# Optimization experiments

Measured on AMD Instinct MI355X. Metric: run time of the kernel, lower is better.

The kernel has to match this reference:

```python
import jax, jax.numpy as jnp
import numpy as np

S, N, LAT, HID, NH, NLAYERS = 8, 128, 128, 384, 8, 6
HT, WT, DT = 128, 128, 128
DIN, DOUT, RAD, LEVELS, FED = 1169, 3 + 3 * 128, 3, 4, 64


def sincos1d(d, pos):
    # MAE-style 1d sincos embedding, d even -> [..., d]
    omega = 1.0 / (10000.0 ** (jnp.arange(d // 2, dtype=jnp.float32) / (d / 2.0)))
    ang = pos[..., None] * omega
    return jnp.concatenate([jnp.sin(ang), jnp.cos(ang)], axis=-1)


def flow_embed(f, Cd=FED):
    # get_3d_embedding(flows, 64, cat_coords=True) -> [..., 3*Cd+3] = 195
    div = jnp.arange(0, Cd, 2, dtype=jnp.float32) * (1000.0 / Cd)
    outs = []
    for a in range(3):
        ang = f[..., a, None] * div
        pe = jnp.stack([jnp.sin(ang), jnp.cos(ang)], axis=-1).reshape(f.shape[:-1] + (Cd,))
        outs.append(pe)
    return jnp.concatenate(outs + [f], axis=-1)


def avg_pool2(x):
    B, Sv, Cc, H, W = x.shape
    return x.reshape(B, Sv, Cc, H // 2, 2, W // 2, 2).mean(axis=(4, 6))


def pyramid(fm):
    pyr = [fm]
    for _ in range(LEVELS - 1):
        fm = avg_pool2(fm)
        pyr.append(fm)
    return pyr


def bilinear_sample(corr, xy):
    # corr: [B,S,N,H,W]; xy: [B,S,N,P,2] pixel coords (x indexes W, y indexes H); zero padding
    B, Sv, Nn, H, W = corr.shape
    cf = corr.reshape(B, Sv, Nn, H * W)
    x, y = xy[..., 0], xy[..., 1]
    x0f = jnp.floor(x); y0f = jnp.floor(y)
    wx, wy = x - x0f, y - y0f
    x0 = x0f.astype(jnp.int32); y0 = y0f.astype(jnp.int32)

    def gather(xi, yi):
        ok = ((xi >= 0) & (xi < W) & (yi >= 0) & (yi < H)).astype(cf.dtype)
        idx = jnp.clip(yi, 0, H - 1) * W + jnp.clip(xi, 0, W - 1)
        v = jnp.take_along_axis(cf, idx.reshape(B, Sv, Nn, -1), axis=-1).reshape(idx.shape)
        return v * ok

    v00 = gather(x0, y0); v01 = gather(x0 + 1, y0)
    v10 = gather(x0, y0 + 1); v11 = gather(x0 + 1, y0 + 1)
    return v00 * (1 - wx) * (1 - wy) + v01 * wx * (1 - wy) + v10 * (1 - wx) * wy + v11 * wx * wy


def corr_sample(pyr, targets, coords):
    # RAFT/CoTracker CorrBlock: per-level dense correlation then (2r+1)^2 window bilinear lookup
    d = jnp.arange(-RAD, RAD + 1, dtype=jnp.float32)
    delta = jnp.stack(jnp.meshgrid(d, d, indexing="ij"), axis=-1).reshape(-1, 2)  # [49,2]
    scale = 1.0 / jnp.sqrt(jnp.float32(targets.shape[-1]))
    outs = []
    for l, fm in enumerate(pyr):
        corr = jnp.einsum("bsnc,bschw->bsnhw", targets, fm) * scale
        xy = coords[..., None, :] / (2.0 ** l) + delta
        outs.append(bilinear_sample(corr, xy))
    return jnp.concatenate(outs, axis=-1)  # [B,S,N,196]


def layernorm(x, g, b):
    m = x.mean(-1, keepdims=True)
    v = x.var(-1, keepdims=True)
    return (x - m) / jnp.sqrt(v + 1e-5) * g + b


def attention(x, Wqkv, bq, Wo, bo):
    M, T, H = x.shape
    dh = H // NH
    qkv = (x @ Wqkv + bq).reshape(M, T, 3, NH, dh)
    q, k, v = qkv[:, :, 0], qkv[:, :, 1], qkv[:, :, 2]
    att = jax.nn.softmax(jnp.einsum("mthd,mshd->mhts", q, k) / jnp.sqrt(jnp.float32(dh)), axis=-1)
    o = jnp.einsum("mhts,mshd->mthd", att, v).reshape(M, T, H)
    return o @ Wo + bo


def updateformer(x, support, W_in, b_in, lnp, Wqkv, bqkv, Wo, bo, W1, b1, W2, b2, W_out, b_out, Ws, bs):
    # x: [B,N,T,DIN]; alternating time (over T) and space (over N) pre-LN transformer blocks
    B, Np, T, _ = x.shape
    sproj = support @ Ws + bs  # [100,HID]
    h = x @ W_in + b_in + sproj.mean(axis=0)
    for i in range(NLAYERS):
        g1, bb1, g2, bb2 = lnp[i, 0], lnp[i, 1], lnp[i, 2], lnp[i, 3]
        if i % 2 == 0:
            y = h.reshape(B * Np, T, HID)
        else:
            y = h.transpose(0, 2, 1, 3).reshape(B * T, Np, HID)
        y = y + attention(layernorm(y, g1, bb1), Wqkv[i], bqkv[i], Wo[i], bo[i])
        z = layernorm(y, g2, bb2)
        y = y + jax.nn.gelu(z @ W1[i] + b1[i], approximate=False) @ W2[i] + b2[i]
        if i % 2 == 0:
            h = y.reshape(B, Np, T, HID)
        else:
            h = y.reshape(B, T, Np, HID).transpose(0, 2, 1, 3)
    return h @ W_out + b_out, sproj[None]


def groupnorm1(x, g, b):
    m = x.mean(-1, keepdims=True)
    v = x.var(-1, keepdims=True)
    return (x - m) / jnp.sqrt(v + 1e-5) * g + b


def _forward(fmapXY, fmapYZ, fmapXZ, coords_init, vis_init, track_mask, feat_init, support_features,
             W_in, b_in, lnp, Wqkv, bqkv, Wo, bo, W1, b1, W2, b2, W_out, b_out, Ws, bs,
             gn_g, gn_b, Wu, bu, Wvis, bvis, iters):
    B, Sv, Cc, H, W = fmapXY.shape
    D = fmapXZ.shape[-2]
    Nn = coords_init.shape[2]
    coords = coords_init
    ffeats = [feat_init[..., k] for k in range(3)]
    pyrXY, pyrYZ, pyrXZ = pyramid(fmapXY), pyramid(fmapYZ), pyramid(fmapXZ)
    grid_size = jnp.array([H, W, D], dtype=jnp.float32)
    # 3d sincos pos embed from query coords; 1169 padded to 1170 -> 390/axis, truncated back
    g = (coords[:, 0] / grid_size * 2.0 - 1.0) * 128.0  # [B,N,3]
    pe = jnp.concatenate([sincos1d(390, g[..., i]) for i in range(3)], axis=-1)[..., :DIN]
    pos_embed = pe.reshape(B * Nn, 1, DIN)
    times_embed = sincos1d(1170, jnp.arange(Sv, dtype=jnp.float32))[None, :, :DIN]
    support = support_features
    for _ in range(iters):
        coords = jax.lax.stop_gradient(coords)  # matches coords.detach()
        fxy = corr_sample(pyrXY, ffeats[0], coords[..., :2])
        fyz = corr_sample(pyrYZ, ffeats[1], coords[..., 1:3])
        fxz = corr_sample(pyrXZ, ffeats[2], coords[..., 0::2])
        fcorrs = jnp.concatenate([fxy, fyz, fxz], axis=-1)  # [B,S,N,588]
        fcorrs_ = fcorrs.transpose(0, 2, 1, 3).reshape(B * Nn, Sv, -1)
        flows_ = (coords - coords[:, :1]).transpose(0, 2, 1, 3).reshape(B * Nn, Sv, 3)
        flows_cat = flow_embed(flows_)  # [BN,S,195]
        ff = [f.transpose(0, 2, 1, 3).reshape(B * Nn, Sv, LAT) for f in ffeats]
        ffeats_ = jnp.concatenate(ff, axis=-1)  # [BN,S,384]
        # replicate torch's cat(dim=2)+permute+reshape layout exactly
        tmv = jnp.concatenate([track_mask, vis_init], axis=2).transpose(0, 2, 1, 3).reshape(B * Nn, Sv, 2)
        tin = jnp.concatenate([flows_cat, fcorrs_, ffeats_, tmv], axis=-1)  # [BN,S,1169]
        x = (tin + pos_embed + times_embed).reshape(B, Nn, Sv, DIN)
        delta, dse3 = updateformer(x, support, W_in, b_in, lnp, Wqkv, bqkv, Wo, bo, W1, b1, W2, b2, W_out, b_out, Ws, bs)
        support = support + dse3[0] / 100.0
        delta = delta.reshape(B * Nn, Sv, DOUT)
        d_coord = delta[..., :3].reshape(B, Nn, Sv, 3).transpose(0, 2, 1, 3)
        coords = coords + d_coord
        new_ffeats = []
        for k in range(3):
            dfk = delta[..., 3 + k * LAT:3 + (k + 1) * LAT]
            upd = jax.nn.gelu(groupnorm1(dfk, gn_g[k], gn_b[k]) @ Wu[k] + bu[k], approximate=False)
            new_ffeats.append(ffeats[k] + upd.reshape(B, Nn, Sv, LAT).transpose(0, 2, 1, 3))
        ffeats = new_ffeats
    vis = (jnp.concatenate(ffeats, axis=-1) @ Wvis + bvis)[..., 0]  # [B,S,N]
    return jnp.concatenate([coords, vis[..., None]], axis=-1)  # [B,S,N,4]


def setup_inputs() -> dict:
    key = jax.random.key(0)
    ks = jax.random.split(key, 16)
    f32 = jnp.float32
    B = 1
    fmapXY = jax.random.normal(ks[0], (B, S, LAT, HT, WT), f32)
    fmapYZ = jax.random.normal(ks[1], (B, S, LAT, DT, HT), f32)
    fmapXZ = jax.random.normal(ks[2], (B, S, LAT, DT, WT), f32)
    coords_init = jax.random.uniform(ks[3], (B, S, N, 3), f32) * 112.0 + 8.0
    vis_init = jnp.ones((B, S, N, 1), f32)
    track_mask = jnp.ones((B, S, N, 1), f32)
    feat_init = jax.random.normal(ks[4], (B, S, N, LAT, 3), f32)
    support_features = jnp.zeros((100, HID), f32) + 0.1
    w = lambda k, sh: jax.random.normal(k, sh, f32) * 0.02
    ln1 = jnp.stack([jnp.ones(HID, f32), jnp.zeros(HID, f32), jnp.ones(HID, f32), jnp.zeros(HID, f32)])
    params = dict(
        W_in=w(ks[5], (DIN, HID)), b_in=jnp.zeros((HID,), f32),
        lnp=jnp.tile(ln1[None], (NLAYERS, 1, 1)),
        Wqkv=w(ks[6], (NLAYERS, HID, 3 * HID)), bqkv=jnp.zeros((NLAYERS, 3 * HID), f32),
        Wo=w(ks[7], (NLAYERS, HID, HID)), bo=jnp.zeros((NLAYERS, HID), f32),
        W1=w(ks[8], (NLAYERS, HID, 4 * HID)), b1=jnp.zeros((NLAYERS, 4 * HID), f32),
        W2=w(ks[9], (NLAYERS, 4 * HID, HID)), b2=jnp.zeros((NLAYERS, HID), f32),
        W_out=w(ks[10], (HID, DOUT)), b_out=jnp.zeros((DOUT,), f32),
        Ws=w(ks[11], (HID, HID)), bs=jnp.zeros((HID,), f32),
        gn_g=jnp.ones((3, LAT), f32), gn_b=jnp.zeros((3, LAT), f32),
        Wu=w(ks[12], (3, LAT, LAT)), bu=jnp.zeros((3, LAT), f32),
        Wvis=w(ks[13], (3 * LAT, 1)), bvis=jnp.zeros((1,), f32),
    )
    return dict(fmapXY=fmapXY, fmapYZ=fmapYZ, fmapXZ=fmapXZ, coords_init=coords_init,
                vis_init=vis_init, track_mask=track_mask, feat_init=feat_init,
                support_features=support_features, iters=2, **params)


def reference(fmapXY, fmapYZ, fmapXZ, coords_init, vis_init, track_mask, feat_init, support_features,
              W_in, b_in, lnp, Wqkv, bqkv, Wo, bo, W1, b1, W2, b2, W_out, b_out, Ws, bs,
              gn_g, gn_b, Wu, bu, Wvis, bvis, iters):
    return _forward(fmapXY, fmapYZ, fmapXZ, coords_init, vis_init, track_mask, feat_init, support_features,
                    W_in, b_in, lnp, Wqkv, bqkv, Wo, bo, W1, b1, W2, b2, W_out, b_out, Ws, bs,
                    gn_g, gn_b, Wu, bu, Wvis, bvis, iters)
```

## Files before the change

### kernel.cpp

```cpp
#include <hip/hip_runtime.h>
#include <hip/hip_bf16.h>


#define DEVFN __device__ __forceinline__

typedef __attribute__((ext_vector_type(8))) short short8;
typedef __attribute__((ext_vector_type(4))) float f32x4;

static constexpr float INV_SQRT_DH = 0.14433756729740643f;
static constexpr float CORR_SCALE  = 0.08838834764831845f;
static constexpr size_t VSTRIDE = 22282240;

DEVFN float gelu_exact(float x){
  return 0.5f * x * (1.0f + erff(x * 0.7071067811865476f));
}
DEVFN short bf16_of(float f){
  __hip_bfloat16 b = __float2bfloat16(f);
  return *reinterpret_cast<short*>(&b);
}


__global__ void init_state_k(float* coords, const float* cinit,
                             float* ff, const float* feat_init,
                             float* support, const float* sfeat){
  int idx = blockIdx.x*256 + threadIdx.x;
  if (idx < 3072)  coords[idx]  = cinit[idx];
  if (idx < 49152){
    int row = idx / 384;
    support[idx] = (row < 100) ? sfeat[idx] : 0.0f;
  }
  if (idx < 393216){
    int k = idx / 131072, rest = idx % 131072;
    ff[idx] = feat_init[(size_t)rest*3 + k];
  }
}

__global__ void build_posE_k(float* posE, const float* cinit){
  int idx = blockIdx.x*256 + threadIdx.x;
  if (idx >= 128*1169) return;
  int n = idx / 1169, d = idx % 1169;
  int i = d / 390, dd = d % 390;
  float c = cinit[n*3 + i];
  float g = (c / 128.0f * 2.0f - 1.0f) * 128.0f;
  int m = (dd < 195) ? dd : dd - 195;
  float om = powf(10000.0f, -(float)m / 195.0f);
  float ang = g * om;
  posE[idx] = (dd < 195) ? sinf(ang) : cosf(ang);
}

__global__ void build_timE_k(float* timE){
  int idx = blockIdx.x*256 + threadIdx.x;
  if (idx >= 8*1169) return;
  int s = idx / 1169, d = idx % 1169;
  int m = (d < 585) ? d : d - 585;
  float om = powf(10000.0f, -(float)m / 585.0f);
  float ang = (float)s * om;
  timE[idx] = (d < 585) ? sinf(ang) : cosf(ang);
}

__global__ void transpose_cl_k(const float* __restrict__ in, __hip_bfloat16* __restrict__ out){
  __shared__ float tile[32][33];
  int s = blockIdx.z;
  int c0 = blockIdx.y*32, h0 = blockIdx.x*32;
  int tx = threadIdx.x & 31, ty = threadIdx.x >> 5;
  const float* ib = in + (size_t)s*128*16384;
  #pragma unroll
  for (int r=0;r<4;r++){
    int c = c0 + ty + r*8;
    tile[ty + r*8][tx] = ib[(size_t)c*16384 + h0 + tx];
  }
  __syncthreads();
  __hip_bfloat16* ob = out + (size_t)s*16384*128;
  #pragma unroll
  for (int r=0;r<4;r++){
    int hw = h0 + ty + r*8;
    ob[(size_t)hw*128 + c0 + tx] = __float2bfloat16(tile[tx][ty + r*8]);
  }
}

__global__ void pool2_k(const __hip_bfloat16* __restrict__ in, __hip_bfloat16* __restrict__ out, int So){
  int idx = blockIdx.x*256 + threadIdx.x;
  int total = 8*So*So*128;
  if (idx >= total) return;
  int c = idx & 127;
  int x = (idx >> 7) % So;
  int y = ((idx >> 7) / So) % So;
  int s = idx / (So*So*128);
  int Si = So*2;
  const __hip_bfloat16* b0 = in + (((size_t)s*Si + 2*y)*Si + 2*x)*128 + c;
  float v = __bfloat162float(b0[0]) + __bfloat162float(b0[128])
          + __bfloat162float(b0[(size_t)Si*128]) + __bfloat162float(b0[(size_t)Si*128 + 128]);
  out[idx] = __float2bfloat16(v*0.25f);
}

__global__ void wtrans_k(const float* __restrict__ in, __hip_bfloat16* __restrict__ out,
                         int K, int N, int Kpad, int Npad){
  __shared__ float tile[32][33];
  int z = blockIdx.z;
  const float* ib = in + (size_t)z*K*N;
  __hip_bfloat16* ob = out + (size_t)z*Npad*Kpad;
  int kb = blockIdx.y*32, nb = blockIdx.x*32;
  int tx = threadIdx.x & 31, ty = threadIdx.x >> 5;
  #pragma unroll
  for (int r=0;r<4;r++){
    int k = kb + ty + r*8, n = nb + tx;
    tile[ty+r*8][tx] = (k < K && n < N) ? ib[(size_t)k*N + n] : 0.0f;
  }
  __syncthreads();
  #pragma unroll
  for (int r=0;r<4;r++){
    int n = nb + ty + r*8, k = kb + tx;
    if (n < Npad && k < Kpad) ob[(size_t)n*Kpad + k] = __float2bfloat16(tile[tx][ty+r*8]);
  }
}

__global__ void corr_k(const __hip_bfloat16* __restrict__ pyr, const float* __restrict__ coords,
                       const float* __restrict__ ff, float* __restrict__ xbuf){
  __shared__ float t[128];
  __shared__ float p[64];
  int bid = blockIdx.x;
  int view = bid >> 10, s = (bid >> 7) & 7, n = bid & 127;
  int tid = threadIdx.x;
  t[tid]      = ff[(size_t)view*131072 + (size_t)(s*128+n)*128 + tid];
  t[tid + 64] = ff[(size_t)view*131072 + (size_t)(s*128+n)*128 + tid + 64];
  int ax = (view==1) ? 1 : 0;
  int ay = (view==0) ? 1 : 2;
  float X = coords[(s*128+n)*3 + ax];
  float Y = coords[(s*128+n)*3 + ay];
  const __hip_bfloat16* vb = pyr + (size_t)view*VSTRIDE;
  __syncthreads();
  size_t loff = 0;
  for (int l=0;l<4;l++){
    int sz = 128 >> l;
    float inv = 1.0f / (float)(1 << l);
    float cx = X * inv, cy = Y * inv;
    float x0f = floorf(cx), y0f = floorf(cy);
    float wx = cx - x0f, wy = cy - y0f;
    int ix0 = (int)x0f, iy0 = (int)y0f;
    int px = ix0 - 3 + (tid & 7);
    int py = iy0 - 3 + (tid >> 3);
    float acc = 0.0f;
    if (px >= 0 && px < sz && py >= 0 && py < sz){
      const uint2* row = reinterpret_cast<const uint2*>(vb + loff + (((size_t)s*sz + py)*sz + px)*128);
      #pragma unroll
      for (int c4=0;c4<32;c4++){
        uint2 u = row[c4];
        float f0 = __uint_as_float(u.x << 16);
        float f1 = __uint_as_float(u.x & 0xffff0000u);
        float f2 = __uint_as_float(u.y << 16);
        float f3 = __uint_as_float(u.y & 0xffff0000u);
        acc += t[c4*4+0]*f0 + t[c4*4+1]*f1 + t[c4*4+2]*f2 + t[c4*4+3]*f3;
      }
    }
    p[tid] = acc;
    __syncthreads();
    if (tid < 49){
      int i = tid / 7, jj = tid % 7;
      float v = p[jj*8+i]       * (1.0f-wx)*(1.0f-wy)
              + p[jj*8+i+1]     * wx*(1.0f-wy)
              + p[(jj+1)*8+i]   * (1.0f-wx)*wy
              + p[(jj+1)*8+i+1] * wx*wy;
      xbuf[(size_t)(n*8+s)*1184 + 195 + view*196 + l*49 + tid] = v * CORR_SCALE;
    }
    loff += (size_t)8*sz*sz*128;
    __syncthreads();
  }
}

__global__ void assemble_x_k(float* __restrict__ xbuf, const float* __restrict__ posE,
                             const float* __restrict__ timE, const float* __restrict__ coords,
                             const float* __restrict__ ff, const float* __restrict__ tmask,
                             const float* __restrict__ vinit){
  int r = blockIdx.x;
  int n = r >> 3, s = r & 7;
  for (int d = threadIdx.x; d < 1184; d += blockDim.x){
    float* dst = xbuf + (size_t)r*1184 + d;
    if (d >= 1169){ *dst = 0.0f; continue; }
    float base = posE[(size_t)n*1169 + d] + timE[(size_t)s*1169 + d];
    if (d >= 195 && d < 783){ *dst += base; continue; }
    float val;
    if (d < 195){
      if (d >= 192){
        int a = d - 192;
        val = coords[(s*128+n)*3 + a] - coords[n*3 + a];
      } else {
        int a = d >> 6, dd = d & 63;
        float f = coords[(s*128+n)*3 + a] - coords[n*3 + a];
        float ang = f * (31.25f * (float)(dd >> 1));
        val = (dd & 1) ? cosf(ang) : sinf(ang);
      }
    } else if (d < 1167){
      int cidx = d - 783, k = cidx >> 7, cc = cidx & 127;
      val = ff[(size_t)k*131072 + (size_t)(s*128+n)*128 + cc];
    } else {
      int c = d - 1167;
      int flat = n*16 + s*2 + c;
      int n2 = flat >> 3, s2 = flat & 7;
      val = (n2 < 128) ? tmask[s2*128 + n2] : vinit[s2*128 + (n2-128)];
    }
    *dst = val + base;
  }
}

__global__ void gn_rows_k(const float* __restrict__ dbuf,
                          const float* __restrict__ gn_g, const float* __restrict__ gn_b,
                          __hip_bfloat16* __restrict__ gtmp){
  int k = blockIdx.y;
  const float* in = dbuf + 3 + k*128;
  const float* g = gn_g + k*128;
  const float* b = gn_b + k*128;
  __hip_bfloat16* out = gtmp + (size_t)k*131072;
  int wave = threadIdx.x >> 6, lane = threadIdx.x & 63;
  int r = blockIdx.x*4 + wave;
  const float* row = in + (size_t)r*387;
  float x0 = row[lane], x1 = row[lane+64];
  float sum = x0 + x1;
  #pragma unroll
  for (int o=32;o>0;o>>=1) sum += __shfl_xor(sum, o);
  float mean = sum / 128.0f;
  float d0 = x0-mean, d1 = x1-mean;
  float vs = d0*d0 + d1*d1;
  #pragma unroll
  for (int o=32;o>0;o>>=1) vs += __shfl_xor(vs, o);
  float invstd = 1.0f / sqrtf(vs/128.0f + 1e-5f);
  out[(size_t)r*128 + lane]      = __float2bfloat16(d0*invstd*g[lane] + b[lane]);
  out[(size_t)r*128 + lane + 64] = __float2bfloat16(d1*invstd*g[lane+64] + b[lane+64]);
}

template<int K, int MODE, bool AF32>
__global__ __launch_bounds__(256) void mgemm_k(const void* __restrict__ A, int lda,
                                               const __hip_bfloat16* __restrict__ Bt,
                                               float* __restrict__ C, int ldc,
                                               int M, int N,
                                               const float* __restrict__ bias,
                                               float* __restrict__ aux){
  constexpr int NSTEP = K/32;
  int tid = threadIdx.x;
  int lane = tid & 63, wid = tid >> 6;
  int wr = wid >> 1, wc = wid & 1;
  int lr = lane & 15, lk = lane >> 4;
  int m0 = blockIdx.y*64 + wr*32;
  int n0 = blockIdx.x*64 + wc*32;

  const __hip_bfloat16* Ab = (const __hip_bfloat16*)A;
  const float* Af = (const float*)A;
  size_t arow0 = (size_t)(m0 + lr)      * lda;
  size_t arow1 = (size_t)(m0 + 16 + lr) * lda;
  size_t brow0 = (size_t)(n0 + lr)      * K;
  size_t brow1 = (size_t)(n0 + 16 + lr) * K;

  f32x4 acc00 = {}, acc01 = {}, acc10 = {}, acc11 = {};

  auto loadAf = [&](size_t rowoff, int k0)->short8{
    if constexpr (AF32){
      const float* p = Af + rowoff + k0 + lk*8;
      short8 r;
      #pragma unroll
      for (int j=0;j<8;j++) r[j] = bf16_of(p[j]);
      return r;
    } else {
      return *reinterpret_cast<const short8*>(Ab + rowoff + k0 + lk*8);
    }
  };
  auto loadBf = [&](size_t rowoff, int k0)->short8{
    return *reinterpret_cast<const short8*>(Bt + rowoff + k0 + lk*8);
  };

  short8 a0 = loadAf(arow0,0), a1 = loadAf(arow1,0);
  short8 b0 = loadBf(brow0,0), b1 = loadBf(brow1,0);
  #pragma unroll
  for (int t=0;t<NSTEP;t++){
    short8 na0={}, na1={}, nb0={}, nb1={};
    if (t+1 < NSTEP){
      int k0 = (t+1)*32;
      na0 = loadAf(arow0,k0); na1 = loadAf(arow1,k0);
      nb0 = loadBf(brow0,k0); nb1 = loadBf(brow1,k0);
    }
    acc00 = __builtin_amdgcn_mfma_f32_16x16x32_bf16(a0,b0,acc00,0,0,0);
    acc01 = __builtin_amdgcn_mfma_f32_16x16x32_bf16(a0,b1,acc01,0,0,0);
    acc10 = __builtin_amdgcn_mfma_f32_16x16x32_bf16(a1,b0,acc10,0,0,0);
    acc11 = __builtin_amdgcn_mfma_f32_16x16x32_bf16(a1,b1,acc11,0,0,0);
    a0=na0; a1=na1; b0=nb0; b1=nb1;
  }

  f32x4 accs[2][2] = {{acc00, acc01},{acc10, acc11}};
  #pragma unroll
  for (int mi=0;mi<2;mi++){
    #pragma unroll
    for (int ni=0;ni<2;ni++){
      int c = n0 + ni*16 + lr;
      if (c >= N) continue;
      float bv = bias ? bias[c] : 0.0f;
      #pragma unroll
      for (int reg=0;reg<4;reg++){
        int r = m0 + mi*16 + lk*4 + reg;
        if (r >= M) continue;
        float v = accs[mi][ni][reg] + bv;
        if (MODE==0) C[(size_t)r*ldc + c] = v;
        else if (MODE==1) C[(size_t)r*ldc + c] += v;
        else {
          int ss = r & 7, nn2 = r >> 3;
          aux[((size_t)(ss*128+nn2))*128 + c] += gelu_exact(v);
        }
      }
    }
  }
}

template<bool GELU>
__global__ __launch_bounds__(256) void lngemm_k(const float* __restrict__ A,
                                                const float* __restrict__ gamma,
                                                const float* __restrict__ beta,
                                                const __hip_bfloat16* __restrict__ Bt,
                                                __hip_bfloat16* __restrict__ Cbf, int ldc, int N,
                                                const float* __restrict__ bias){
  constexpr int LDSS = 392;
  __shared__ short Asm[64*LDSS];
  int tid = threadIdx.x, lane = tid & 63, w = tid >> 6;
  int m0 = blockIdx.y*64, n0b = blockIdx.x*64;

  float gg[6], bb[6];
  #pragma unroll
  for (int e=0;e<6;e++){ gg[e] = gamma[lane+e*64]; bb[e] = beta[lane+e*64]; }
  for (int rr=0; rr<16; rr++){
    int r = w*16 + rr;
    const float* row = A + (size_t)(m0+r)*384;
    float x[6]; float sum = 0.0f;
    #pragma unroll
    for (int e=0;e<6;e++){ x[e] = row[lane+e*64]; sum += x[e]; }
    #pragma unroll
    for (int o=32;o>0;o>>=1) sum += __shfl_xor(sum, o);
    float mean = sum * (1.0f/384.0f);
    float vs = 0.0f;
    #pragma unroll
    for (int e=0;e<6;e++){ float d = x[e]-mean; vs += d*d; }
    #pragma unroll
    for (int o=32;o>0;o>>=1) vs += __shfl_xor(vs, o);
    float invstd = 1.0f / sqrtf(vs*(1.0f/384.0f) + 1e-5f);
    #pragma unroll
    for (int e=0;e<6;e++)
      Asm[r*LDSS + lane + e*64] = bf16_of((x[e]-mean)*invstd*gg[e] + bb[e]);
  }
  __syncthreads();

  int wr = w >> 1, wc = w & 1;
  int lr = lane & 15, lk = lane >> 4;
  const __hip_bfloat16* Brow0 = Bt + (size_t)(n0b + wc*32 + lr)*384;
  const __hip_bfloat16* Brow1 = Brow0 + 16*384;
  short8 b0 = *(const short8*)(Brow0 + lk*8);
  short8 b1 = *(const short8*)(Brow1 + lk*8);
  f32x4 acc00={}, acc01={}, acc10={}, acc11={};
  #pragma unroll
  for (int t=0;t<12;t++){
    short8 a0 = *(const short8*)(&Asm[(wr*32+lr)*LDSS    + t*32 + lk*8]);
    short8 a1 = *(const short8*)(&Asm[(wr*32+16+lr)*LDSS + t*32 + lk*8]);
    short8 nb0={}, nb1={};
    if (t < 11){
      nb0 = *(const short8*)(Brow0 + (t+1)*32 + lk*8);
      nb1 = *(const short8*)(Brow1 + (t+1)*32 + lk*8);
    }
    acc00 = __builtin_amdgcn_mfma_f32_16x16x32_bf16(a0,b0,acc00,0,0,0);
    acc01 = __builtin_amdgcn_mfma_f32_16x16x32_bf16(a0,b1,acc01,0,0,0);
    acc10 = __builtin_amdgcn_mfma_f32_16x16x32_bf16(a1,b0,acc10,0,0,0);
    acc11 = __builtin_amdgcn_mfma_f32_16x16x32_bf16(a1,b1,acc11,0,0,0);
    b0=nb0; b1=nb1;
  }
  f32x4 accs[2][2] = {{acc00, acc01},{acc10, acc11}};
  #pragma unroll
  for (int mi=0;mi<2;mi++){
    #pragma unroll
    for (int ni=0;ni<2;ni++){
      int c = n0b + wc*32 + ni*16 + lr;
      float bv = bias[c];
      #pragma unroll
      for (int reg=0;reg<4;reg++){
        int r = m0 + wr*32 + mi*16 + lk*4 + reg;
        float v = accs[mi][ni][reg] + bv;
        Cbf[(size_t)r*ldc + c] = __float2bfloat16(GELU ? gelu_exact(v) : v);
      }
    }
  }
}

__global__ __launch_bounds__(256) void wu_gemm_k(const __hip_bfloat16* __restrict__ gtmp,
                                                 const __hip_bfloat16* __restrict__ WuT,
                                                 const float* __restrict__ bu,
                                                 float* __restrict__ ff){
  int z = blockIdx.z;
  const __hip_bfloat16* A  = gtmp + (size_t)z*131072;
  const __hip_bfloat16* Bt = WuT  + (size_t)z*16384;
  const float* bias = bu + (size_t)z*128;
  float* aux = ff + (size_t)z*131072;
  int tid = threadIdx.x, lane = tid & 63, wid = tid >> 6;
  int wr = wid >> 1, wc = wid & 1;
  int lr = lane & 15, lk = lane >> 4;
  int m0 = blockIdx.y*64 + wr*32;
  int n0 = blockIdx.x*64 + wc*32;
  const short8* A0 = (const short8*)(A + (size_t)(m0+lr)*128);
  const short8* A1 = (const short8*)(A + (size_t)(m0+16+lr)*128);
  const short8* B0 = (const short8*)(Bt + (size_t)(n0+lr)*128);
  const short8* B1 = (const short8*)(Bt + (size_t)(n0+16+lr)*128);
  f32x4 acc00={}, acc01={}, acc10={}, acc11={};
  #pragma unroll
  for (int t=0;t<4;t++){
    short8 a0 = A0[t*4 + lk], a1 = A1[t*4 + lk];
    short8 b0 = B0[t*4 + lk], b1 = B1[t*4 + lk];
    acc00 = __builtin_amdgcn_mfma_f32_16x16x32_bf16(a0,b0,acc00,0,0,0);
    acc01 = __builtin_amdgcn_mfma_f32_16x16x32_bf16(a0,b1,acc01,0,0,0);
    acc10 = __builtin_amdgcn_mfma_f32_16x16x32_bf16(a1,b0,acc10,0,0,0);
    acc11 = __builtin_amdgcn_mfma_f32_16x16x32_bf16(a1,b1,acc11,0,0,0);
  }
  f32x4 accs[2][2] = {{acc00, acc01},{acc10, acc11}};
  #pragma unroll
  for (int mi=0;mi<2;mi++){
    #pragma unroll
    for (int ni=0;ni<2;ni++){
      int c = n0 + ni*16 + lr;
      float bv = bias[c];
      #pragma unroll
      for (int reg=0;reg<4;reg++){
        int r = m0 + mi*16 + lk*4 + reg;
        float v = accs[mi][ni][reg] + bv;
        int ss = r & 7, nn2 = r >> 3;
        aux[((size_t)(ss*128+nn2))*128 + c] += gelu_exact(v);
      }
    }
  }
}

DEVFN void load48bf(const __hip_bfloat16* p, float* q){
  const uint32_t* u = (const uint32_t*)p;
  #pragma unroll
  for (int i=0;i<24;i++){
    uint32_t w = u[i];
    q[2*i]   = __uint_as_float(w << 16);
    q[2*i+1] = __uint_as_float(w & 0xffff0000u);
  }
}

__global__ void attn_even_k(const __hip_bfloat16* __restrict__ qkv, __hip_bfloat16* __restrict__ attout){
  int g = blockIdx.x;
  int tid = threadIdx.x;
  int h = tid >> 3, t = tid & 7;
  float q[48];
  load48bf(qkv + (size_t)(g*8+t)*1152 + h*48, q);
  float sc[8]; float mx = -1e30f;
  #pragma unroll
  for (int j=0;j<8;j++){
    float kr[48];
    load48bf(qkv + (size_t)(g*8+j)*1152 + 384 + h*48, kr);
    float sum = 0.0f;
    #pragma unroll
    for (int d=0;d<48;d++) sum += q[d]*kr[d];
    sum *= INV_SQRT_DH;
    sc[j] = sum; mx = fmaxf(mx, sum);
  }
  float l = 0.0f;
  #pragma unroll
  for (int j=0;j<8;j++){ sc[j] = expf(sc[j]-mx); l += sc[j]; }
  float o[48];
  #pragma unroll
  for (int d=0;d<48;d++) o[d] = 0.0f;
  #pragma unroll
  for (int j=0;j<8;j++){
    float vr[48];
    load48bf(qkv + (size_t)(g*8+j)*1152 + 768 + h*48, vr);
    float pj = sc[j];
    #pragma unroll
    for (int d=0;d<48;d++) o[d] += pj*vr[d];
  }
  float invl = 1.0f/l;
  __hip_bfloat16* orow = attout + (size_t)(g*8+t)*384 + h*48;
  #pragma unroll
  for (int d=0;d<48;d++) orow[d] = __float2bfloat16(o[d]*invl);
}

__global__ __launch_bounds__(256) void attn_odd_mfma_k(const __hip_bfloat16* __restrict__ qkv,
                                                       __hip_bfloat16* __restrict__ attout){
  __shared__ char smem[47872];
  short* Qb = (short*)smem;
  short* Kb = (short*)(smem + 18432);
  short* Pb = (short*)smem;
  short* Vt = (short*)(smem + 34816);
  int g = blockIdx.x & 7, h = blockIdx.x >> 3;
  int tid = threadIdx.x;

  const short* qs = (const short*)qkv;
  for (int idx = tid; idx < 768; idx += 256){
    int t = idx / 6, dblk = idx % 6;
    size_t base = (size_t)(t*8+g)*1152 + h*48 + dblk*8;
    *(short8*)(Qb + t*72 + dblk*8) = *(const short8*)(qs + base);
    *(short8*)(Kb + t*72 + dblk*8) = *(const short8*)(qs + base + 384);
  }
  short8 zz = {};
  for (int idx = tid; idx < 384; idx += 256){
    int t = idx / 3, dblk = idx % 3;
    *(short8*)(Qb + t*72 + 48 + dblk*8) = zz;
    *(short8*)(Kb + t*72 + 48 + dblk*8) = zz;
  }
  __syncthreads();

  int lane = tid & 63, w = tid >> 6;
  int lr = lane & 15, lk = lane >> 4;
  int m0 = w*32;

  f32x4 S[2][8] = {};
  #pragma unroll
  for (int ks=0; ks<2; ks++){
    short8 a0 = *(const short8*)(Qb + (m0+lr)*72    + ks*32 + lk*8);
    short8 a1 = *(const short8*)(Qb + (m0+16+lr)*72 + ks*32 + lk*8);
    #pragma unroll
    for (int ni=0; ni<8; ni++){
      short8 b = *(const short8*)(Kb + (ni*16+lr)*72 + ks*32 + lk*8);
      S[0][ni] = __builtin_amdgcn_mfma_f32_16x16x32_bf16(a0,b,S[0][ni],0,0,0);
      S[1][ni] = __builtin_amdgcn_mfma_f32_16x16x32_bf16(a1,b,S[1][ni],0,0,0);
    }
  }

  #pragma unroll
  for (int mi=0;mi<2;mi++){
    #pragma unroll
    for (int reg=0;reg<4;reg++){
      float m = -1e30f;
      #pragma unroll
      for (int ni=0;ni<8;ni++) m = fmaxf(m, S[mi][ni][reg]);
      #pragma unroll
      for (int o=1;o<16;o<<=1) m = fmaxf(m, __shfl_xor(m, o));
      m *= INV_SQRT_DH;
      float l = 0.0f;
      #pragma unroll
      for (int ni=0;ni<8;ni++){
        float p = expf(S[mi][ni][reg]*INV_SQRT_DH - m);
        S[mi][ni][reg] = p;
        l += p;
      }
      #pragma unroll
      for (int o=1;o<16;o<<=1) l += __shfl_xor(l, o);
      float inv = 1.0f/l;
      #pragma unroll
      for (int ni=0;ni<8;ni++) S[mi][ni][reg] *= inv;
    }
  }
  __syncthreads();

  for (int idx = tid; idx < 768; idx += 256){
    int j = idx / 6, dblk = idx % 6;
    short8 v = *(const short8*)(qs + (size_t)(j*8+g)*1152 + 768 + h*48 + dblk*8);
    #pragma unroll
    for (int e=0;e<8;e++) Vt[(dblk*8+e)*136 + j] = v[e];
  }
  #pragma unroll
  for (int mi=0;mi<2;mi++)
    #pragma unroll
    for (int ni=0;ni<8;ni++)
      #pragma unroll
      for (int reg=0;reg<4;reg++)
        Pb[(m0+mi*16+lk*4+reg)*136 + ni*16+lr] = bf16_of(S[mi][ni][reg]);
  __syncthreads();

  f32x4 O[2][3] = {};
  #pragma unroll
  for (int ks=0; ks<4; ks++){
    short8 a0 = *(const short8*)(Pb + (m0+lr)*136    + ks*32 + lk*8);
    short8 a1 = *(const short8*)(Pb + (m0+16+lr)*136 + ks*32 + lk*8);
    #pragma unroll
    for (int ni=0; ni<3; ni++){
      short8 b = *(const short8*)(Vt + (ni*16+lr)*136 + ks*32 + lk*8);
      O[0][ni] = __builtin_amdgcn_mfma_f32_16x16x32_bf16(a0,b,O[0][ni],0,0,0);
      O[1][ni] = __builtin_amdgcn_mfma_f32_16x16x32_bf16(a1,b,O[1][ni],0,0,0);
    }
  }
  #pragma unroll
  for (int mi=0;mi<2;mi++){
    #pragma unroll
    for (int ni=0;ni<3;ni++){
      #pragma unroll
      for (int reg=0;reg<4;reg++){
        int q = m0 + mi*16 + lk*4 + reg;
        int d = ni*16 + lr;
        attout[(size_t)(q*8+g)*384 + h*48 + d] = __float2bfloat16(O[mi][ni][reg]);
      }
    }
  }
}

__global__ void supp_smean_k(const float* __restrict__ sproj, const float* __restrict__ b_in,
                             float* __restrict__ bias2, float* __restrict__ support){
  int idx = blockIdx.x*256 + threadIdx.x;
  if (idx < 38400) support[idx] += sproj[idx]*0.01f;
  else if (idx < 38784){
    int c = idx - 38400;
    float s = 0.0f;
    for (int r=0;r<100;r++) s += sproj[r*384 + c];
    bias2[c] = b_in[c] + s*0.01f;
  }
}

__global__ void coords_upd_k(float* coords, const float* dbuf){
  int idx = blockIdx.x*256 + threadIdx.x;
  if (idx >= 3072) return;
  int a = idx % 3, sn = idx / 3;
  int s = sn >> 7, n = sn & 127;
  coords[idx] += dbuf[(size_t)(n*8+s)*387 + a];
}

__global__ void final_out_k(const float* __restrict__ coords, const float* __restrict__ ff,
                            const float* __restrict__ Wvis, const float* __restrict__ bvis,
                            float* __restrict__ out){
  int sn = blockIdx.x*64 + threadIdx.x;
  if (sn >= 1024) return;
  float acc = bvis[0];
  for (int k=0;k<3;k++)
    for (int c=0;c<128;c++)
      acc += ff[(size_t)k*131072 + (size_t)sn*128 + c] * Wvis[k*128 + c];
  out[sn*4+0] = coords[sn*3+0];
  out[sn*4+1] = coords[sn*3+1];
  out[sn*4+2] = coords[sn*3+2];
  out[sn*4+3] = acc;
}


extern "C" void kernel_launch(void* const* d_in, const int* in_sizes, int n_in,
                              void* d_out, int out_size, void* d_ws, size_t ws_size,
                              hipStream_t stream) {
  const float* fmapXY   = (const float*)d_in[0];
  const float* fmapYZ   = (const float*)d_in[1];
  const float* fmapXZ   = (const float*)d_in[2];
  const float* cinit    = (const float*)d_in[3];
  const float* vinit    = (const float*)d_in[4];
  const float* tmask    = (const float*)d_in[5];
  const float* feat_init= (const float*)d_in[6];
  const float* sfeat    = (const float*)d_in[7];
  const float* W_in     = (const float*)d_in[9];
  const float* b_in     = (const float*)d_in[10];
  const float* lnp      = (const float*)d_in[11];
  const float* Wqkv     = (const float*)d_in[12];
  const float* bqkv     = (const float*)d_in[13];
  const float* Wo       = (const float*)d_in[14];
  const float* bo       = (const float*)d_in[15];
  const float* W1       = (const float*)d_in[16];
  const float* b1       = (const float*)d_in[17];
  const float* W2       = (const float*)d_in[18];
  const float* b2       = (const float*)d_in[19];
  const float* W_out    = (const float*)d_in[20];
  const float* b_out    = (const float*)d_in[21];
  const float* Ws       = (const float*)d_in[22];
  const float* bs       = (const float*)d_in[23];
  const float* gn_g     = (const float*)d_in[24];
  const float* gn_b     = (const float*)d_in[25];
  const float* Wu       = (const float*)d_in[26];
  const float* bu       = (const float*)d_in[27];
  const float* Wvis     = (const float*)d_in[28];
  const float* bvis     = (const float*)d_in[29];
  const int ITERS = 2;

  char* wp = (char*)d_ws;
  auto alloc = [&](size_t bytes)->char* {
    char* p = wp; wp += (bytes + 255) & ~(size_t)255; return p;
  };
  __hip_bfloat16* pyr = (__hip_bfloat16*)alloc(3ull*VSTRIDE*2);
  float* coords = (float*)alloc(3072ull*4);
  float* ff     = (float*)alloc(393216ull*4);
  float* support= (float*)alloc(49152ull*4);
  float* sproj  = (float*)alloc(38400ull*4);
  float* bias2  = (float*)alloc(384ull*4);
  float* posE   = (float*)alloc(149632ull*4);
  float* timE   = (float*)alloc(9352ull*4);
  float* xbuf   = (float*)alloc(1212416ull*4);
  float* h      = (float*)alloc(393216ull*4);
  float* dbuf   = (float*)alloc(396288ull*4);
  __hip_bfloat16* qkv_bf  = (__hip_bfloat16*)alloc(1179648ull*2);
  __hip_bfloat16* atto_bf = (__hip_bfloat16*)alloc(393216ull*2);
  __hip_bfloat16* ffb_bf  = (__hip_bfloat16*)alloc(1572864ull*2);
  __hip_bfloat16* gtmp_bf = (__hip_bfloat16*)alloc(393216ull*2);
  __hip_bfloat16* WsT   = (__hip_bfloat16*)alloc(147456ull*2);
  __hip_bfloat16* WinT  = (__hip_bfloat16*)alloc(454656ull*2);
  __hip_bfloat16* WqkvT = (__hip_bfloat16*)alloc(2654208ull*2);
  __hip_bfloat16* WoT   = (__hip_bfloat16*)alloc(884736ull*2);
  __hip_bfloat16* W1T   = (__hip_bfloat16*)alloc(3538944ull*2);
  __hip_bfloat16* W2T   = (__hip_bfloat16*)alloc(3538944ull*2);
  __hip_bfloat16* WoutT = (__hip_bfloat16*)alloc(172032ull*2);
  __hip_bfloat16* WuT   = (__hip_bfloat16*)alloc(49152ull*2);
  if ((size_t)(wp - (char*)d_ws) > ws_size) return;

  init_state_k<<<1536, 256, 0, stream>>>(coords, cinit, ff, feat_init, support, sfeat);
  build_posE_k<<<(128*1169 + 255)/256, 256, 0, stream>>>(posE, cinit);
  build_timE_k<<<(8*1169 + 255)/256, 256, 0, stream>>>(timE);

  const float* fmaps[3] = {fmapXY, fmapYZ, fmapXZ};
  for (int v=0; v<3; v++){
    __hip_bfloat16* base = pyr + (size_t)v*VSTRIDE;
    transpose_cl_k<<<dim3(512,4,8), 256, 0, stream>>>(fmaps[v], base);
    pool2_k<<<(8*64*64*128 + 255)/256, 256, 0, stream>>>(base,              base + 16777216, 64);
    pool2_k<<<(8*32*32*128 + 255)/256, 256, 0, stream>>>(base + 16777216,   base + 20971520, 32);
    pool2_k<<<(8*16*16*128 + 255)/256, 256, 0, stream>>>(base + 20971520,   base + 22020096, 16);
  }

  wtrans_k<<<dim3(12,12,1), 256, 0, stream>>>(Ws,    WsT,   384, 384, 384, 384);
  wtrans_k<<<dim3(12,37,1), 256, 0, stream>>>(W_in,  WinT,  1169,384, 1184,384);
  wtrans_k<<<dim3(36,12,6), 256, 0, stream>>>(Wqkv,  WqkvT, 384, 1152,384, 1152);
  wtrans_k<<<dim3(12,12,6), 256, 0, stream>>>(Wo,    WoT,   384, 384, 384, 384);
  wtrans_k<<<dim3(48,12,6), 256, 0, stream>>>(W1,    W1T,   384, 1536,384, 1536);
  wtrans_k<<<dim3(12,48,6), 256, 0, stream>>>(W2,    W2T,   1536,384, 1536,384);
  wtrans_k<<<dim3(14,12,1), 256, 0, stream>>>(W_out, WoutT, 384, 387, 384, 448);
  wtrans_k<<<dim3(4,4,3),   256, 0, stream>>>(Wu,    WuT,   128, 128, 128, 128);

  for (int it=0; it<ITERS; ++it){
    corr_k<<<3072, 64, 0, stream>>>(pyr, coords, ff, xbuf);
    assemble_x_k<<<1024, 256, 0, stream>>>(xbuf, posE, timE, coords, ff, tmask, vinit);

    mgemm_k<384,0,true><<<dim3(6,2), 256, 0, stream>>>(support,384, WsT, sproj,384, 100,384, bs, nullptr);
    supp_smean_k<<<152, 256, 0, stream>>>(sproj, b_in, bias2, support);

    mgemm_k<1184,0,true><<<dim3(6,16), 256, 0, stream>>>(xbuf,1184, WinT, h,384, 1024,384, bias2, nullptr);

    for (int i=0;i<6;i++){
      const float* g1  = lnp + (size_t)(i*4+0)*384;
      const float* bb1 = lnp + (size_t)(i*4+1)*384;
      const float* g2  = lnp + (size_t)(i*4+2)*384;
      const float* bb2 = lnp + (size_t)(i*4+3)*384;

      lngemm_k<false><<<dim3(18,16), 256, 0, stream>>>(h, g1, bb1, WqkvT + (size_t)i*442368,
                                                       qkv_bf, 1152, 1152, bqkv + i*1152);
      if ((i & 1) == 0) attn_even_k<<<128, 64, 0, stream>>>(qkv_bf, atto_bf);
      else              attn_odd_mfma_k<<<64, 256, 0, stream>>>(qkv_bf, atto_bf);
      mgemm_k<384,1,false><<<dim3(6,16), 256, 0, stream>>>(atto_bf,384, WoT + (size_t)i*147456,
                                                           h,384, 1024,384, bo + i*384, nullptr);
      lngemm_k<true><<<dim3(24,16), 256, 0, stream>>>(h, g2, bb2, W1T + (size_t)i*589824,
                                                      ffb_bf, 1536, 1536, b1 + i*1536);
      mgemm_k<1536,1,false><<<dim3(6,16), 256, 0, stream>>>(ffb_bf,1536, W2T + (size_t)i*589824,
                                                            h,384, 1024,384, b2 + i*384, nullptr);
    }

    mgemm_k<384,0,true><<<dim3(7,16), 256, 0, stream>>>(h,384, WoutT, dbuf,387, 1024,387, b_out, nullptr);
    coords_upd_k<<<12, 256, 0, stream>>>(coords, dbuf);

    gn_rows_k<<<dim3(256,3), 256, 0, stream>>>(dbuf, gn_g, gn_b, gtmp_bf);
    wu_gemm_k<<<dim3(2,16,3), 256, 0, stream>>>(gtmp_bf, WuT, bu, ff);
  }

  final_out_k<<<16, 64, 0, stream>>>(coords, ff, Wvis, bvis, (float*)d_out);
}
```

Baseline: 1.545 ms.

## Store input activations in bf16, parallelize even attention, fold coords update into GN

The input activation buffer is now stored in bf16. The assemble step runs before the correlation kernel, and corr_k adds its result in place, so the input GEMM reads bf16 directly instead of converting fp32 on load. The even-layer attention kernel is rewritten to use 512 threads per block, with one lane per query-key pair and shuffle-based softmax, replacing a 64-thread per-query loop. The coordinate update is folded into the group-norm kernel to remove a launch. The read-modify-write in bf16 adds extra rounding to the correlation features.

```diff
diff --git a/kernel.cpp b/kernel.cpp
--- a/kernel.cpp
+++ b/kernel.cpp
@@ -18,6 +18,7 @@
   __hip_bfloat16 b = __float2bfloat16(f);
   return *reinterpret_cast<short*>(&b);
 }
+DEVFN float bfu(uint32_t u16){ return __uint_as_float(u16 << 16); }
 
 
 __global__ void init_state_k(float* coords, const float* cinit,
@@ -114,8 +115,43 @@
   }
 }
 
+__global__ void assemble_x_k(__hip_bfloat16* __restrict__ xbuf, const float* __restrict__ posE,
+                             const float* __restrict__ timE, const float* __restrict__ coords,
+                             const float* __restrict__ ff, const float* __restrict__ tmask,
+                             const float* __restrict__ vinit){
+  int r = blockIdx.x;
+  int n = r >> 3, s = r & 7;
+  for (int d = threadIdx.x; d < 1184; d += blockDim.x){
+    __hip_bfloat16* dst = xbuf + (size_t)r*1184 + d;
+    if (d >= 1169){ *dst = __float2bfloat16(0.0f); continue; }
+    float base = posE[(size_t)n*1169 + d] + timE[(size_t)s*1169 + d];
+    if (d >= 195 && d < 783){ *dst = __float2bfloat16(base); continue; }
+    float val;
+    if (d < 195){
+      if (d >= 192){
+        int a = d - 192;
+        val = coords[(s*128+n)*3 + a] - coords[n*3 + a];
+      } else {
+        int a = d >> 6, dd = d & 63;
+        float f = coords[(s*128+n)*3 + a] - coords[n*3 + a];
+        float ang = f * (31.25f * (float)(dd >> 1));
+        val = (dd & 1) ? cosf(ang) : sinf(ang);
+      }
+    } else if (d < 1167){
+      int cidx = d - 783, k = cidx >> 7, cc = cidx & 127;
+      val = ff[(size_t)k*131072 + (size_t)(s*128+n)*128 + cc];
+    } else {
+      int c = d - 1167;
+      int flat = n*16 + s*2 + c;
+      int n2 = flat >> 3, s2 = flat & 7;
+      val = (n2 < 128) ? tmask[s2*128 + n2] : vinit[s2*128 + (n2-128)];
+    }
+    *dst = __float2bfloat16(val + base);
+  }
+}
+
 __global__ void corr_k(const __hip_bfloat16* __restrict__ pyr, const float* __restrict__ coords,
-                       const float* __restrict__ ff, float* __restrict__ xbuf){
+                       const float* __restrict__ ff, __hip_bfloat16* __restrict__ xbuf){
   __shared__ float t[128];
   __shared__ float p[64];
   int bid = blockIdx.x;
@@ -160,51 +196,17 @@
               + p[jj*8+i+1]     * wx*(1.0f-wy)
               + p[(jj+1)*8+i]   * (1.0f-wx)*wy
               + p[(jj+1)*8+i+1] * wx*wy;
-      xbuf[(size_t)(n*8+s)*1184 + 195 + view*196 + l*49 + tid] = v * CORR_SCALE;
+      __hip_bfloat16* dst = xbuf + (size_t)(n*8+s)*1184 + 195 + view*196 + l*49 + tid;
+      *dst = __float2bfloat16(__bfloat162float(*dst) + v * CORR_SCALE);
     }
     loff += (size_t)8*sz*sz*128;
     __syncthreads();
   }
 }
 
-__global__ void assemble_x_k(float* __restrict__ xbuf, const float* __restrict__ posE,
-                             const float* __restrict__ timE, const float* __restrict__ coords,
-                             const float* __restrict__ ff, const float* __restrict__ tmask,
-                             const float* __restrict__ vinit){
-  int r = blockIdx.x;
-  int n = r >> 3, s = r & 7;
-  for (int d = threadIdx.x; d < 1184; d += blockDim.x){
-    float* dst = xbuf + (size_t)r*1184 + d;
-    if (d >= 1169){ *dst = 0.0f; continue; }
-    float base = posE[(size_t)n*1169 + d] + timE[(size_t)s*1169 + d];
-    if (d >= 195 && d < 783){ *dst += base; continue; }
-    float val;
-    if (d < 195){
-      if (d >= 192){
-        int a = d - 192;
-        val = coords[(s*128+n)*3 + a] - coords[n*3 + a];
-      } else {
-        int a = d >> 6, dd = d & 63;
-        float f = coords[(s*128+n)*3 + a] - coords[n*3 + a];
-        float ang = f * (31.25f * (float)(dd >> 1));
-        val = (dd & 1) ? cosf(ang) : sinf(ang);
-      }
-    } else if (d < 1167){
-      int cidx = d - 783, k = cidx >> 7, cc = cidx & 127;
-      val = ff[(size_t)k*131072 + (size_t)(s*128+n)*128 + cc];
-    } else {
-      int c = d - 1167;
-      int flat = n*16 + s*2 + c;
-      int n2 = flat >> 3, s2 = flat & 7;
-      val = (n2 < 128) ? tmask[s2*128 + n2] : vinit[s2*128 + (n2-128)];
-    }
-    *dst = val + base;
-  }
-}
-
 __global__ void gn_rows_k(const float* __restrict__ dbuf,
                           const float* __restrict__ gn_g, const float* __restrict__ gn_b,
-                          __hip_bfloat16* __restrict__ gtmp){
+                          __hip_bfloat16* __restrict__ gtmp, float* __restrict__ coords){
   int k = blockIdx.y;
   const float* in = dbuf + 3 + k*128;
   const float* g = gn_g + k*128;
@@ -225,6 +227,14 @@
   float invstd = 1.0f / sqrtf(vs/128.0f + 1e-5f);
   out[(size_t)r*128 + lane]      = __float2bfloat16(d0*invstd*g[lane] + b[lane]);
   out[(size_t)r*128 + lane + 64] = __float2bfloat16(d1*invstd*g[lane+64] + b[lane+64]);
+  if (k == 0 && blockIdx.x < 12){
+    int idx = blockIdx.x*256 + threadIdx.x;
+    if (idx < 3072){
+      int a = idx % 3, sn = idx / 3;
+      int ss = sn >> 7, nn = sn & 127;
+      coords[idx] += dbuf[(size_t)(nn*8+ss)*387 + a];
+    }
+  }
 }
 
 template<int K, int MODE, bool AF32>
@@ -232,8 +242,7 @@
                                                const __hip_bfloat16* __restrict__ Bt,
                                                float* __restrict__ C, int ldc,
                                                int M, int N,
-                                               const float* __restrict__ bias,
-                                               float* __restrict__ aux){
+                                               const float* __restrict__ bias){
   constexpr int NSTEP = K/32;
   int tid = threadIdx.x;
   int lane = tid & 63, wid = tid >> 6;
@@ -297,11 +306,7 @@
         if (r >= M) continue;
         float v = accs[mi][ni][reg] + bv;
         if (MODE==0) C[(size_t)r*ldc + c] = v;
-        else if (MODE==1) C[(size_t)r*ldc + c] += v;
-        else {
-          int ss = r & 7, nn2 = r >> 3;
-          aux[((size_t)(ss*128+nn2))*128 + c] += gelu_exact(v);
-        }
+        else C[(size_t)r*ldc + c] += v;
       }
     }
   }
@@ -428,51 +433,56 @@
   }
 }
 
-DEVFN void load48bf(const __hip_bfloat16* p, float* q){
-  const uint32_t* u = (const uint32_t*)p;
-  #pragma unroll
-  for (int i=0;i<24;i++){
-    uint32_t w = u[i];
-    q[2*i]   = __uint_as_float(w << 16);
-    q[2*i+1] = __uint_as_float(w & 0xffff0000u);
-  }
-}
-
-__global__ void attn_even_k(const __hip_bfloat16* __restrict__ qkv, __hip_bfloat16* __restrict__ attout){
+__global__ __launch_bounds__(512) void attn_even_k(const __hip_bfloat16* __restrict__ qkv,
+                                                   __hip_bfloat16* __restrict__ attout){
   int g = blockIdx.x;
-  int tid = threadIdx.x;
-  int h = tid >> 3, t = tid & 7;
-  float q[48];
-  load48bf(qkv + (size_t)(g*8+t)*1152 + h*48, q);
-  float sc[8]; float mx = -1e30f;
-  #pragma unroll
-  for (int j=0;j<8;j++){
-    float kr[48];
-    load48bf(qkv + (size_t)(g*8+j)*1152 + 384 + h*48, kr);
-    float sum = 0.0f;
-    #pragma unroll
-    for (int d=0;d<48;d++) sum += q[d]*kr[d];
-    sum *= INV_SQRT_DH;
-    sc[j] = sum; mx = fmaxf(mx, sum);
-  }
-  float l = 0.0f;
-  #pragma unroll
-  for (int j=0;j<8;j++){ sc[j] = expf(sc[j]-mx); l += sc[j]; }
-  float o[48];
-  #pragma unroll
-  for (int d=0;d<48;d++) o[d] = 0.0f;
-  #pragma unroll
-  for (int j=0;j<8;j++){
-    float vr[48];
-    load48bf(qkv + (size_t)(g*8+j)*1152 + 768 + h*48, vr);
-    float pj = sc[j];
-    #pragma unroll
-    for (int d=0;d<48;d++) o[d] += pj*vr[d];
-  }
-  float invl = 1.0f/l;
-  __hip_bfloat16* orow = attout + (size_t)(g*8+t)*384 + h*48;
-  #pragma unroll
-  for (int d=0;d<48;d++) orow[d] = __float2bfloat16(o[d]*invl);
+  int h = threadIdx.x >> 6;
+  int lane = threadIdx.x & 63;
+  int t = lane >> 3, j = lane & 7;
+  const short* qs = (const short*)qkv;
+
+  float q[48], kk[48];
+  {
+    const short8* qp = (const short8*)(qs + (size_t)(g*8+t)*1152 + h*48);
+    const short8* kp = (const short8*)(qs + (size_t)(g*8+j)*1152 + 384 + h*48);
+    #pragma unroll
+    for (int c=0;c<6;c++){
+      short8 qv = qp[c], kv = kp[c];
+      #pragma unroll
+      for (int e=0;e<8;e++){
+        q[c*8+e]  = bfu((uint16_t)qv[e]);
+        kk[c*8+e] = bfu((uint16_t)kv[e]);
+      }
+    }
+  }
+  float s = 0.0f;
+  #pragma unroll
+  for (int d=0;d<48;d++) s += q[d]*kk[d];
+  s *= INV_SQRT_DH;
+  float mx = s;
+  #pragma unroll
+  for (int o=1;o<8;o<<=1) mx = fmaxf(mx, __shfl_xor(mx, o));
+  float e = expf(s - mx);
+  float l = e;
+  #pragma unroll
+  for (int o=1;o<8;o<<=1) l += __shfl_xor(l, o);
+  float p = e / l;
+
+  float o6[6] = {0,0,0,0,0,0};
+  #pragma unroll
+  for (int jp=0;jp<8;jp++){
+    float pj = __shfl(p, (lane & 56) | jp);
+    const uint32_t* vp = (const uint32_t*)(qs + (size_t)(g*8+jp)*1152 + 768 + h*48 + j*6);
+    uint32_t w0 = vp[0], w1 = vp[1], w2 = vp[2];
+    o6[0] += pj * bfu(w0 & 0xffffu); o6[1] += pj * bfu(w0 >> 16);
+    o6[2] += pj * bfu(w1 & 0xffffu); o6[3] += pj * bfu(w1 >> 16);
+    o6[4] += pj * bfu(w2 & 0xffffu); o6[5] += pj * bfu(w2 >> 16);
+  }
+  uint32_t r0 = ((uint32_t)(uint16_t)bf16_of(o6[1]) << 16) | (uint16_t)bf16_of(o6[0]);
+  uint32_t r1 = ((uint32_t)(uint16_t)bf16_of(o6[3]) << 16) | (uint16_t)bf16_of(o6[2]);
+  uint32_t r2 = ((uint32_t)(uint16_t)bf16_of(o6[5]) << 16) | (uint16_t)bf16_of(o6[4]);
+  uint32_t* op = (uint32_t*)((short*)attout + (size_t)(g*8+t)*384 + h*48 + j*6);
+  op[0] = r0; op[1] = r1; op[2] = r2;
 }
 
 __global__ __launch_bounds__(256) void attn_odd_mfma_k(const __hip_bfloat16* __restrict__ qkv,
@@ -594,14 +604,6 @@
     for (int r=0;r<100;r++) s += sproj[r*384 + c];
     bias2[c] = b_in[c] + s*0.01f;
   }
-}
-
-__global__ void coords_upd_k(float* coords, const float* dbuf){
-  int idx = blockIdx.x*256 + threadIdx.x;
-  if (idx >= 3072) return;
-  int a = idx % 3, sn = idx / 3;
-  int s = sn >> 7, n = sn & 127;
-  coords[idx] += dbuf[(size_t)(n*8+s)*387 + a];
 }
 
 __global__ void final_out_k(const float* __restrict__ coords, const float* __restrict__ ff,
@@ -666,9 +668,9 @@
   float* bias2  = (float*)alloc(384ull*4);
   float* posE   = (float*)alloc(149632ull*4);
   float* timE   = (float*)alloc(9352ull*4);
-  float* xbuf   = (float*)alloc(1212416ull*4);
   float* h      = (float*)alloc(393216ull*4);
   float* dbuf   = (float*)alloc(396288ull*4);
+  __hip_bfloat16* xbuf_bf = (__hip_bfloat16*)alloc(1212416ull*2);
   __hip_bfloat16* qkv_bf  = (__hip_bfloat16*)alloc(1179648ull*2);
   __hip_bfloat16* atto_bf = (__hip_bfloat16*)alloc(393216ull*2);
   __hip_bfloat16* ffb_bf  = (__hip_bfloat16*)alloc(1572864ull*2);
@@ -706,13 +708,13 @@
   wtrans_k<<<dim3(4,4,3),   256, 0, stream>>>(Wu,    WuT,   128, 128, 128, 128);
 
   for (int it=0; it<ITERS; ++it){
-    corr_k<<<3072, 64, 0, stream>>>(pyr, coords, ff, xbuf);
-    assemble_x_k<<<1024, 256, 0, stream>>>(xbuf, posE, timE, coords, ff, tmask, vinit);
-
-    mgemm_k<384,0,true><<<dim3(6,2), 256, 0, stream>>>(support,384, WsT, sproj,384, 100,384, bs, nullptr);
+    assemble_x_k<<<1024, 256, 0, stream>>>(xbuf_bf, posE, timE, coords, ff, tmask, vinit);
+    corr_k<<<3072, 64, 0, stream>>>(pyr, coords, ff, xbuf_bf);
+
+    mgemm_k<384,0,true><<<dim3(6,2), 256, 0, stream>>>(support,384, WsT, sproj,384, 100,384, bs);
     supp_smean_k<<<152, 256, 0, stream>>>(sproj, b_in, bias2, support);
 
-    mgemm_k<1184,0,true><<<dim3(6,16), 256, 0, stream>>>(xbuf,1184, WinT, h,384, 1024,384, bias2, nullptr);
+    mgemm_k<1184,0,false><<<dim3(6,16), 256, 0, stream>>>(xbuf_bf,1184, WinT, h,384, 1024,384, bias2);
 
     for (int i=0;i<6;i++){
       const float* g1  = lnp + (size_t)(i*4+0)*384;
@@ -722,20 +724,18 @@
 
       lngemm_k<false><<<dim3(18,16), 256, 0, stream>>>(h, g1, bb1, WqkvT + (size_t)i*442368,
                                                        qkv_bf, 1152, 1152, bqkv + i*1152);
-      if ((i & 1) == 0) attn_even_k<<<128, 64, 0, stream>>>(qkv_bf, atto_bf);
+      if ((i & 1) == 0) attn_even_k<<<128, 512, 0, stream>>>(qkv_bf, atto_bf);
       else              attn_odd_mfma_k<<<64, 256, 0, stream>>>(qkv_bf, atto_bf);
       mgemm_k<384,1,false><<<dim3(6,16), 256, 0, stream>>>(atto_bf,384, WoT + (size_t)i*147456,
-                                                           h,384, 1024,384, bo + i*384, nullptr);
+                                                           h,384, 1024,384, bo + i*384);
       lngemm_k<true><<<dim3(24,16), 256, 0, stream>>>(h, g2, bb2, W1T + (size_t)i*589824,
                                                       ffb_bf, 1536, 1536, b1 + i*1536);
       mgemm_k<1536,1,false><<<dim3(6,16), 256, 0, stream>>>(ffb_bf,1536, W2T + (size_t)i*589824,
-                                                            h,384, 1024,384, b2 + i*384, nullptr);
-    }
-
-    mgemm_k<384,0,true><<<dim3(7,16), 256, 0, stream>>>(h,384, WoutT, dbuf,387, 1024,387, b_out, nullptr);
-    coords_upd_k<<<12, 256, 0, stream>>>(coords, dbuf);
-
-    gn_rows_k<<<dim3(256,3), 256, 0, stream>>>(dbuf, gn_g, gn_b, gtmp_bf);
+                                                            h,384, 1024,384, b2 + i*384);
+    }
+
+    mgemm_k<384,0,true><<<dim3(7,16), 256, 0, stream>>>(h,384, WoutT, dbuf,387, 1024,387, b_out);
+    gn_rows_k<<<dim3(256,3), 256, 0, stream>>>(dbuf, gn_g, gn_b, gtmp_bf, coords);
     wu_gemm_k<<<dim3(2,16,3), 256, 0, stream>>>(gtmp_bf, WuT, bu, ff);
   }
 
```

After: 1.451 ms. 6.1% less time.
